# Performance work log

Hardware: AMD Instinct MI355X
Metric: run time of the kernel (lower is better)

Reference implementation:

```python
import jax, jax.numpy as jnp
import numpy as np

N_NODES = 100000
N_EDGES = 1600000
DIM_IN = 128
DIM_OUT = 64


def _spmm(edge_row, edge_col, edge_vals, X):
    # DAD.mm(X): sparse COO [N,N] times dense [N,d]
    # gather source features, scale by edge value, scatter-add to rows
    msgs = edge_vals[:, None] * X[edge_col]          # [E, d]
    return jax.ops.segment_sum(msgs, edge_row, num_segments=N_NODES)


def setup_inputs() -> dict:
    key = jax.random.key(0)
    k1, k2, k3, k4, k5, k6 = jax.random.split(key, 6)
    X = jax.random.normal(k1, (N_NODES, DIM_IN), dtype=jnp.float32)
    W1 = jax.random.normal(k2, (DIM_IN, DIM_IN), dtype=jnp.float32) * (1.0 / np.sqrt(DIM_IN))
    W2 = jax.random.normal(k3, (DIM_OUT, DIM_IN), dtype=jnp.float32) * (1.0 / np.sqrt(DIM_IN))
    edge_vals = jax.random.uniform(k4, (N_EDGES,), dtype=jnp.float32)
    edge_row = jax.random.randint(k5, (N_EDGES,), 0, N_NODES, dtype=jnp.int32)
    edge_col = jax.random.randint(k6, (N_EDGES,), 0, N_NODES, dtype=jnp.int32)
    return {"X": X, "W1": W1, "W2": W2, "edge_vals": edge_vals,
            "edge_row": edge_row, "edge_col": edge_col}


def reference(X, W1, W2, edge_vals, edge_row, edge_col):
    # layer 1: tanh(fc1(DAD @ X)); nn.Linear(bias=False) is x @ W.T
    h = jnp.tanh(_spmm(edge_row, edge_col, edge_vals, X) @ W1.T)
    # layer 2: tanh(fc2(DAD @ h))
    out = jnp.tanh(_spmm(edge_row, edge_col, edge_vals, h) @ W2.T)
    return out
```

## Files before the change

kernel.cpp:

```cpp
#include <hip/hip_runtime.h>
#include <hip/hip_bf16.h>
#include <hip/hip_fp16.h>

#define N_NODES 100000
#define N_EDGES 1600000
#define DIM_IN 128
#define DIM_OUT 64

#define NB 391
#define NCHUNK 391
#define CHUNK 4096
#define BCAP 5120
#define EPCAP 6144

typedef unsigned int uint;
typedef unsigned short ushort;
typedef _Float16 half8 __attribute__((ext_vector_type(8)));
typedef float f32x4 __attribute__((ext_vector_type(4)));

__device__ inline ushort f2h(float f) {
    __half h = __float2half(f);
    return *reinterpret_cast<ushort*>(&h);
}


__global__ __launch_bounds__(256) void chunk_hist_kernel(const int* __restrict__ erow,
                                                         int* __restrict__ counts, int E) {
    __shared__ int hist[NB];
    const int t = threadIdx.x, c = blockIdx.x;
    for (int b = t; b < NB; b += 256) hist[b] = 0;
    __syncthreads();
    const int eb = c * CHUNK;
#pragma unroll
    for (int i = 0; i < CHUNK / 256; ++i) {
        int e = eb + i * 256 + t;
        if (e < E) atomicAdd(&hist[erow[e] >> 8], 1);
    }
    __syncthreads();
    for (int b = t; b < NB; b += 256) counts[b * NCHUNK + c] = hist[b];
}

__global__ __launch_bounds__(512) void bucket_scan_kernel(const int* __restrict__ counts,
                                                          int* __restrict__ offnb,
                                                          int* __restrict__ tot) {
    __shared__ int s[512];
    const int b = blockIdx.x, t = threadIdx.x;
    int v = (t < NCHUNK) ? counts[b * NCHUNK + t] : 0;
    s[t] = v;
    __syncthreads();
#pragma unroll
    for (int o = 1; o < 512; o <<= 1) {
        int x = s[t];
        int y = (t >= o) ? s[t - o] : 0;
        __syncthreads();
        s[t] = x + y;
        __syncthreads();
    }
    if (t < NCHUNK) offnb[b * NCHUNK + t] = s[t] - v;
    if (t == 511) tot[b] = s[511];
}

__global__ __launch_bounds__(512) void base_scan_kernel(const int* __restrict__ tot,
                                                        int* __restrict__ bbase) {
    __shared__ int s[512];
    const int t = threadIdx.x;
    int v = (t < NB) ? tot[t] : 0;
    s[t] = v;
    __syncthreads();
#pragma unroll
    for (int o = 1; o < 512; o <<= 1) {
        int x = s[t];
        int y = (t >= o) ? s[t - o] : 0;
        __syncthreads();
        s[t] = x + y;
        __syncthreads();
    }
    if (t < NB) bbase[t] = s[t] - v;
    if (t == 511) bbase[NB] = s[511];
}

__global__ __launch_bounds__(512) void coarse_scatter_kernel(const int* __restrict__ erow,
                                                             const int* __restrict__ ecol,
                                                             const float* __restrict__ eval,
                                                             const int* __restrict__ offnb,
                                                             const int* __restrict__ bbase,
                                                             uint* __restrict__ keyOut,
                                                             float* __restrict__ valOut, int E) {
    __shared__ int hist[NB];
    __shared__ int segOff[NB];
    __shared__ int localOff[NB];
    __shared__ int sc[512];
    __shared__ int idxL[CHUNK];
    __shared__ int gaddrL[CHUNK];

    const int t = threadIdx.x, c = blockIdx.x;
    for (int b = t; b < NB; b += 512) {
        hist[b] = 0;
        segOff[b] = bbase[b] + offnb[b * NCHUNK + c];
    }
    __syncthreads();
    const int eb = c * CHUNK;
    uint bq[CHUNK / 512];
#pragma unroll
    for (int i = 0; i < CHUNK / 512; ++i) {
        int e = eb + i * 512 + t;
        if (e < E) {
            int b = erow[e] >> 8;
            int q = atomicAdd(&hist[b], 1);
            bq[i] = ((uint)b << 16) | (uint)q;
        } else {
            bq[i] = 0xFFFFFFFFu;
        }
    }
    __syncthreads();
    int v = (t < NB) ? hist[t] : 0;
    sc[t] = v;
    __syncthreads();
#pragma unroll
    for (int o = 1; o < 512; o <<= 1) {
        int x = sc[t];
        int y = (t >= o) ? sc[t - o] : 0;
        __syncthreads();
        sc[t] = x + y;
        __syncthreads();
    }
    if (t < NB) localOff[t] = sc[t] - v;
    __syncthreads();
#pragma unroll
    for (int i = 0; i < CHUNK / 512; ++i) {
        if (bq[i] != 0xFFFFFFFFu) {
            int b = bq[i] >> 16;
            int q = bq[i] & 0xFFFF;
            int s = localOff[b] + q;
            idxL[s] = eb + i * 512 + t;
            gaddrL[s] = segOff[b] + q;
        }
    }
    __syncthreads();
    const int m = min(CHUNK, E - eb);
    for (int s = t; s < m; s += 512) {
        int e = idxL[s];
        int g = gaddrL[s];
        keyOut[g] = ((uint)(erow[e] & 255) << 17) | (uint)ecol[e];
        valOut[g] = eval[e];
    }
}

__global__ __launch_bounds__(256) void fine_sort_kernel(const uint* __restrict__ keyOut,
                                                        const float* __restrict__ valOut,
                                                        const int* __restrict__ bbase,
                                                        int* __restrict__ row_ptr,
                                                        int* __restrict__ row_len,
                                                        int2* __restrict__ ep) {
    __shared__ uint keyL[BCAP];
    __shared__ int hist[256];
    __shared__ int offs[256];
    const int b = blockIdx.x, t = threadIdx.x;
    const int s0 = bbase[b], s1 = bbase[b + 1];
    const int m = min(s1 - s0, BCAP);
    hist[t] = 0;
    __syncthreads();
    for (int j = t; j < m; j += 256) {
        uint k = keyOut[s0 + j];
        keyL[j] = k;
        atomicAdd(&hist[k >> 17], 1);
    }
    __syncthreads();
    const int deg = hist[t];
    const int pdeg = (deg + 7) & ~7;
    offs[t] = pdeg;
    __syncthreads();
#pragma unroll
    for (int o = 1; o < 256; o <<= 1) {
        int x = offs[t];
        int y = (t >= o) ? offs[t - o] : 0;
        __syncthreads();
        offs[t] = x + y;
        __syncthreads();
    }
    const int pexcl = offs[t] - pdeg;
    const int base = b * EPCAP;
    const int row = b * 256 + t;
    if (row < N_NODES) {
        row_ptr[row] = base + pexcl;
        row_len[row] = pdeg;
    }
    hist[t] = pexcl;
    __syncthreads();
    for (int j = t; j < m; j += 256) {
        uint k = keyL[j];
        int pos = atomicAdd(&hist[k >> 17], 1);
        ep[base + pos] = make_int2((int)(k & 0x1FFFFu), __float_as_int(valOut[s0 + j]));
    }
    __syncthreads();
    for (int j = pexcl + deg; j < pexcl + pdeg; ++j)
        ep[base + j] = make_int2(0, 0);
}


__global__ __launch_bounds__(256) void cvt_f16_kernel(const float* __restrict__ in,
                                                      uint* __restrict__ outp, int n8) {
    int i = blockIdx.x * 256 + threadIdx.x;
    if (i >= n8) return;
    const float4* in4 = reinterpret_cast<const float4*>(in) + (size_t)i * 2;
    float4 a = in4[0];
    float4 b = in4[1];
    uint4 o;
    o.x = (uint)f2h(a.x) | ((uint)f2h(a.y) << 16);
    o.y = (uint)f2h(a.z) | ((uint)f2h(a.w) << 16);
    o.z = (uint)f2h(b.x) | ((uint)f2h(b.y) << 16);
    o.w = (uint)f2h(b.z) | ((uint)f2h(b.w) << 16);
    reinterpret_cast<uint4*>(outp)[i] = o;
}


template <int NOUT, bool TANH, bool AF32>
__global__ __launch_bounds__(256) void mfma_gemm_kernel(const void* __restrict__ Ain,
                                                        const uint* __restrict__ Wh,
                                                        uint* __restrict__ Out, int M) {
    constexpr int CF = NOUT / 16;
    __shared__ __align__(16) ushort sA[128 * 128];
    __shared__ __align__(16) ushort sB[NOUT * 128];

    const int t = threadIdx.x;
    const int l = t & 63;
    const int w = t >> 6;
    const int row0 = blockIdx.x * 128;
    const int lr = l & 15;
    const int lk = l >> 4;

    if (AF32) {
        const float* Af = (const float*)Ain;
#pragma unroll
        for (int i = 0; i < 16; ++i) {
            int fid = i * 256 + t;
            int row = fid >> 5, q4 = fid & 31;
            int gr = row0 + row;
            float4 v = make_float4(0.f, 0.f, 0.f, 0.f);
            if (gr < M) v = *reinterpret_cast<const float4*>(Af + (size_t)gr * 128 + q4 * 4);
            uint2 p;
            p.x = (uint)f2h(v.x) | ((uint)f2h(v.y) << 16);
            p.y = (uint)f2h(v.z) | ((uint)f2h(v.w) << 16);
            int slot = q4 >> 1;
            *reinterpret_cast<uint2*>(&sA[row * 128 + ((slot ^ (row & 7)) << 3) + (q4 & 1) * 4]) = p;
        }
    } else {
        const uint4* A4 = (const uint4*)Ain;
#pragma unroll
        for (int i = 0; i < 8; ++i) {
            int fid = i * 256 + t;
            int row = fid >> 4, slot = fid & 15;
            int gr = row0 + row;
            uint4 v = make_uint4(0, 0, 0, 0);
            if (gr < M) v = A4[(size_t)gr * 16 + slot];
            *reinterpret_cast<uint4*>(&sA[row * 128 + ((slot ^ (row & 7)) << 3)]) = v;
        }
    }
#pragma unroll
    for (int i = 0; i < NOUT / 16; ++i) {
        int fid = i * 256 + t;
        int row = fid >> 4, slot = fid & 15;
        uint4 v = reinterpret_cast<const uint4*>(Wh)[row * 16 + slot];
        *reinterpret_cast<uint4*>(&sB[row * 128 + ((slot ^ (row & 7)) << 3)]) = v;
    }
    __syncthreads();

    f32x4 acc[2][CF];
#pragma unroll
    for (int rf = 0; rf < 2; ++rf)
#pragma unroll
        for (int cf = 0; cf < CF; ++cf) acc[rf][cf] = (f32x4){0.f, 0.f, 0.f, 0.f};

    half8 aF[2][4];
#pragma unroll
    for (int rf = 0; rf < 2; ++rf) {
        int row = w * 32 + rf * 16 + lr;
#pragma unroll
        for (int kc = 0; kc < 4; ++kc) {
            int slot = kc * 4 + lk;
            aF[rf][kc] = *reinterpret_cast<const half8*>(&sA[row * 128 + ((slot ^ (row & 7)) << 3)]);
        }
    }
#pragma unroll
    for (int cf = 0; cf < CF; ++cf) {
        int col = cf * 16 + lr;
#pragma unroll
        for (int kc = 0; kc < 4; ++kc) {
            int slot = kc * 4 + lk;
            half8 bF = *reinterpret_cast<const half8*>(&sB[col * 128 + ((slot ^ (col & 7)) << 3)]);
            acc[0][cf] = __builtin_amdgcn_mfma_f32_16x16x32_f16(aF[0][kc], bF, acc[0][cf], 0, 0, 0);
            acc[1][cf] = __builtin_amdgcn_mfma_f32_16x16x32_f16(aF[1][kc], bF, acc[1][cf], 0, 0, 0);
        }
    }
    __syncthreads();

    ushort* sOut = sA;
#pragma unroll
    for (int rf = 0; rf < 2; ++rf)
#pragma unroll
        for (int cf = 0; cf < CF; ++cf)
#pragma unroll
            for (int reg = 0; reg < 4; ++reg) {
                int row = w * 32 + rf * 16 + lk * 4 + reg;
                int col = cf * 16 + lr;
                float x = acc[rf][cf][reg];
                sOut[row * NOUT + col] = f2h(TANH ? tanhf(x) : x);
            }
    __syncthreads();
    constexpr int QPR = NOUT / 8;
#pragma unroll
    for (int i = 0; i < 128 * QPR / 256; ++i) {
        int fid = i * 256 + t;
        int row = fid / QPR, q = fid % QPR;
        int gr = row0 + row;
        if (gr < M)
            reinterpret_cast<uint4*>(Out)[(size_t)gr * QPR + q] =
                *reinterpret_cast<const uint4*>(&sOut[row * NOUT + q * 8]);
    }
}


__global__ __launch_bounds__(256) void spmm1_kernel(const int2* __restrict__ ep,
                                                    const int* __restrict__ row_ptr,
                                                    const int* __restrict__ row_len,
                                                    const uint* __restrict__ T,
                                                    uint* __restrict__ Hh) {
    int wave = threadIdx.x >> 6;
    int lane = threadIdx.x & 63;
    int r = blockIdx.x * 4 + wave;
    if (r >= N_NODES) return;
    int beg = row_ptr[r];
    int end = beg + row_len[r];
    float a0x = 0.f, a0y = 0.f, a1x = 0.f, a1y = 0.f;
    for (int e = beg; e < end; e += 8) {
        int2 cv[8];
        uint xu[8];
#pragma unroll
        for (int i = 0; i < 8; ++i) cv[i] = ep[e + i];
#pragma unroll
        for (int i = 0; i < 8; ++i) xu[i] = T[(size_t)cv[i].x * 64 + lane];
#pragma unroll
        for (int i = 0; i < 8; ++i) {
            float v = __int_as_float(cv[i].y);
            __half2 h2 = *reinterpret_cast<__half2*>(&xu[i]);
            float2 f = __half22float2(h2);
            if (i & 1) { a1x += v * f.x; a1y += v * f.y; }
            else       { a0x += v * f.x; a0y += v * f.y; }
        }
    }
    Hh[(size_t)r * 64 + lane] =
        (uint)f2h(tanhf(a0x + a1x)) | ((uint)f2h(tanhf(a0y + a1y)) << 16);
}


__global__ __launch_bounds__(256) void spmm2_kernel(const int2* __restrict__ ep,
                                                    const int* __restrict__ row_ptr,
                                                    const int* __restrict__ row_len,
                                                    const ushort* __restrict__ Ph,
                                                    float* __restrict__ out) {
    int wave = threadIdx.x >> 6;
    int lane = threadIdx.x & 63;
    int r = blockIdx.x * 4 + wave;
    if (r >= N_NODES) return;
    int beg = row_ptr[r];
    int end = beg + row_len[r];
    float acc0 = 0.f, acc1 = 0.f;
    for (int e = beg; e < end; e += 8) {
        int2 cv[8];
        ushort xu[8];
#pragma unroll
        for (int i = 0; i < 8; ++i) cv[i] = ep[e + i];
#pragma unroll
        for (int i = 0; i < 8; ++i) xu[i] = Ph[(size_t)cv[i].x * 64 + lane];
#pragma unroll
        for (int i = 0; i < 8; ++i) {
            float v = __int_as_float(cv[i].y);
            __half h = *reinterpret_cast<__half*>(&xu[i]);
            float x = __half2float(h);
            if (i & 1) acc1 += v * x;
            else       acc0 += v * x;
        }
    }
    out[(size_t)r * DIM_OUT + lane] = tanhf(acc0 + acc1);
}


extern "C" void kernel_launch(void* const* d_in, const int* in_sizes, int n_in,
                              void* d_out, int out_size, void* d_ws, size_t ws_size,
                              hipStream_t stream) {
    const float* X = (const float*)d_in[0];
    const float* W1 = (const float*)d_in[1];
    const float* W2 = (const float*)d_in[2];
    const float* evals = (const float*)d_in[3];
    const int* erow = (const int*)d_in[4];
    const int* ecol = (const int*)d_in[5];
    float* out = (float*)d_out;

    const int N = N_NODES;
    const int E = N_EDGES;

    char* ws = (char*)d_ws;
    size_t off = 0;
    auto alloc = [&](size_t bytes) {
        size_t o = off;
        off = (off + bytes + 255) & ~(size_t)255;
        return o;
    };
    size_t o_counts = alloc((size_t)NB * NCHUNK * 4);
    size_t o_offnb = alloc((size_t)NB * NCHUNK * 4);
    size_t o_tot = alloc((size_t)NB * 4);
    size_t o_bbase = alloc((size_t)(NB + 1) * 4);
    size_t o_rowptr = alloc((size_t)N * 4);
    size_t o_rowlen = alloc((size_t)N * 4);
    size_t o_ep = alloc((size_t)NB * EPCAP * 8);
    size_t o_key = alloc((size_t)E * 4);
    size_t o_val = alloc((size_t)E * 4);
    size_t o_xw1 = alloc((size_t)N * 64 * 4);
    size_t o_hh = alloc((size_t)N * 64 * 4);
    size_t o_ph = alloc((size_t)N * 32 * 4);
    size_t o_w1h = alloc((size_t)128 * 64 * 4);
    size_t o_w2h = alloc((size_t)64 * 64 * 4);
    (void)ws_size;

    int* counts = (int*)(ws + o_counts);
    int* offnb = (int*)(ws + o_offnb);
    int* tot = (int*)(ws + o_tot);
    int* bbase = (int*)(ws + o_bbase);
    int* row_ptr = (int*)(ws + o_rowptr);
    int* row_len = (int*)(ws + o_rowlen);
    int2* ep = (int2*)(ws + o_ep);
    uint* keyOut = (uint*)(ws + o_key);
    float* valOut = (float*)(ws + o_val);
    uint* XW1h = (uint*)(ws + o_xw1);
    uint* Hh = (uint*)(ws + o_hh);
    uint* Ph = (uint*)(ws + o_ph);
    uint* W1h = (uint*)(ws + o_w1h);
    uint* W2h = (uint*)(ws + o_w2h);

    const int gemm_grid = (N + 127) / 128;
    const int spmm_grid = (N + 3) / 4;

    cvt_f16_kernel<<<8, 256, 0, stream>>>(W1, W1h, 128 * 128 / 8);
    cvt_f16_kernel<<<4, 256, 0, stream>>>(W2, W2h, 64 * 128 / 8);
    mfma_gemm_kernel<128, false, true><<<gemm_grid, 256, 0, stream>>>(X, W1h, XW1h, N);

    chunk_hist_kernel<<<NCHUNK, 256, 0, stream>>>(erow, counts, E);
    bucket_scan_kernel<<<NB, 512, 0, stream>>>(counts, offnb, tot);
    base_scan_kernel<<<1, 512, 0, stream>>>(tot, bbase);
    coarse_scatter_kernel<<<NCHUNK, 512, 0, stream>>>(erow, ecol, evals, offnb, bbase,
                                                      keyOut, valOut, E);
    fine_sort_kernel<<<NB, 256, 0, stream>>>(keyOut, valOut, bbase, row_ptr, row_len, ep);

    spmm1_kernel<<<spmm_grid, 256, 0, stream>>>(ep, row_ptr, row_len, XW1h, Hh);
    mfma_gemm_kernel<64, false, false><<<gemm_grid, 256, 0, stream>>>(Hh, W2h, Ph, N);
    spmm2_kernel<<<spmm_grid, 256, 0, stream>>>(ep, row_ptr, row_len, (const ushort*)Ph, out);
}
```

Before: 208.1 us.

## Fuse first SpMM with second-layer GEMM and merge weight conversions

The first SpMM kernel now processes 16 rows per block, writes the tanh'd rows into shared memory, and immediately multiplies them by W2 with MFMA. This removes the Hh intermediate round trip to global memory and one GEMM launch. The two weight-conversion kernels are merged into one launch, and the GEMM is specialised to the 128-output case. Each block now also loads all of W2 into shared memory, and the larger blocks may lower occupancy or balance load less evenly across rows of different degree.

```diff
diff --git a/kernel.cpp b/kernel.cpp
--- a/kernel.cpp
+++ b/kernel.cpp
@@ -198,11 +198,18 @@
 }
 
 
-__global__ __launch_bounds__(256) void cvt_f16_kernel(const float* __restrict__ in,
-                                                      uint* __restrict__ outp, int n8) {
+__global__ __launch_bounds__(256) void cvt_weights_kernel(const float* __restrict__ W1,
+                                                          const float* __restrict__ W2,
+                                                          uint* __restrict__ W1h,
+                                                          uint* __restrict__ W2h) {
     int i = blockIdx.x * 256 + threadIdx.x;
-    if (i >= n8) return;
-    const float4* in4 = reinterpret_cast<const float4*>(in) + (size_t)i * 2;
+    const float* in;
+    uint* outp;
+    int j;
+    if (i < 2048) { in = W1; outp = W1h; j = i; }
+    else if (i < 3072) { in = W2; outp = W2h; j = i - 2048; }
+    else return;
+    const float4* in4 = reinterpret_cast<const float4*>(in) + (size_t)j * 2;
     float4 a = in4[0];
     float4 b = in4[1];
     uint4 o;
@@ -210,17 +217,15 @@
     o.y = (uint)f2h(a.z) | ((uint)f2h(a.w) << 16);
     o.z = (uint)f2h(b.x) | ((uint)f2h(b.y) << 16);
     o.w = (uint)f2h(b.z) | ((uint)f2h(b.w) << 16);
-    reinterpret_cast<uint4*>(outp)[i] = o;
-}
-
-
-template <int NOUT, bool TANH, bool AF32>
-__global__ __launch_bounds__(256) void mfma_gemm_kernel(const void* __restrict__ Ain,
-                                                        const uint* __restrict__ Wh,
-                                                        uint* __restrict__ Out, int M) {
-    constexpr int CF = NOUT / 16;
+    reinterpret_cast<uint4*>(outp)[j] = o;
+}
+
+
+__global__ __launch_bounds__(256) void mfma_gemm128_kernel(const float* __restrict__ Af,
+                                                           const uint* __restrict__ Wh,
+                                                           uint* __restrict__ Out, int M) {
     __shared__ __align__(16) ushort sA[128 * 128];
-    __shared__ __align__(16) ushort sB[NOUT * 128];
+    __shared__ __align__(16) ushort sB[128 * 128];
 
     const int t = threadIdx.x;
     const int l = t & 63;
@@ -229,35 +234,21 @@
     const int lr = l & 15;
     const int lk = l >> 4;
 
-    if (AF32) {
-        const float* Af = (const float*)Ain;
-#pragma unroll
-        for (int i = 0; i < 16; ++i) {
-            int fid = i * 256 + t;
-            int row = fid >> 5, q4 = fid & 31;
-            int gr = row0 + row;
-            float4 v = make_float4(0.f, 0.f, 0.f, 0.f);
-            if (gr < M) v = *reinterpret_cast<const float4*>(Af + (size_t)gr * 128 + q4 * 4);
-            uint2 p;
-            p.x = (uint)f2h(v.x) | ((uint)f2h(v.y) << 16);
-            p.y = (uint)f2h(v.z) | ((uint)f2h(v.w) << 16);
-            int slot = q4 >> 1;
-            *reinterpret_cast<uint2*>(&sA[row * 128 + ((slot ^ (row & 7)) << 3) + (q4 & 1) * 4]) = p;
-        }
-    } else {
-        const uint4* A4 = (const uint4*)Ain;
-#pragma unroll
-        for (int i = 0; i < 8; ++i) {
-            int fid = i * 256 + t;
-            int row = fid >> 4, slot = fid & 15;
-            int gr = row0 + row;
-            uint4 v = make_uint4(0, 0, 0, 0);
-            if (gr < M) v = A4[(size_t)gr * 16 + slot];
-            *reinterpret_cast<uint4*>(&sA[row * 128 + ((slot ^ (row & 7)) << 3)]) = v;
-        }
-    }
-#pragma unroll
-    for (int i = 0; i < NOUT / 16; ++i) {
+#pragma unroll
+    for (int i = 0; i < 16; ++i) {
+        int fid = i * 256 + t;
+        int row = fid >> 5, q4 = fid & 31;
+        int gr = row0 + row;
+        float4 v = make_float4(0.f, 0.f, 0.f, 0.f);
+        if (gr < M) v = *reinterpret_cast<const float4*>(Af + (size_t)gr * 128 + q4 * 4);
+        uint2 p;
+        p.x = (uint)f2h(v.x) | ((uint)f2h(v.y) << 16);
+        p.y = (uint)f2h(v.z) | ((uint)f2h(v.w) << 16);
+        int slot = q4 >> 1;
+        *reinterpret_cast<uint2*>(&sA[row * 128 + ((slot ^ (row & 7)) << 3) + (q4 & 1) * 4]) = p;
+    }
+#pragma unroll
+    for (int i = 0; i < 8; ++i) {
         int fid = i * 256 + t;
         int row = fid >> 4, slot = fid & 15;
         uint4 v = reinterpret_cast<const uint4*>(Wh)[row * 16 + slot];
@@ -265,11 +256,11 @@
     }
     __syncthreads();
 
-    f32x4 acc[2][CF];
+    f32x4 acc[2][8];
 #pragma unroll
     for (int rf = 0; rf < 2; ++rf)
 #pragma unroll
-        for (int cf = 0; cf < CF; ++cf) acc[rf][cf] = (f32x4){0.f, 0.f, 0.f, 0.f};
+        for (int cf = 0; cf < 8; ++cf) acc[rf][cf] = (f32x4){0.f, 0.f, 0.f, 0.f};
 
     half8 aF[2][4];
 #pragma unroll
@@ -282,7 +273,7 @@
         }
     }
 #pragma unroll
-    for (int cf = 0; cf < CF; ++cf) {
+    for (int cf = 0; cf < 8; ++cf) {
         int col = cf * 16 + lr;
 #pragma unroll
         for (int kc = 0; kc < 4; ++kc) {
@@ -298,58 +289,106 @@
 #pragma unroll
     for (int rf = 0; rf < 2; ++rf)
 #pragma unroll
-        for (int cf = 0; cf < CF; ++cf)
+        for (int cf = 0; cf < 8; ++cf)
 #pragma unroll
             for (int reg = 0; reg < 4; ++reg) {
                 int row = w * 32 + rf * 16 + lk * 4 + reg;
                 int col = cf * 16 + lr;
-                float x = acc[rf][cf][reg];
-                sOut[row * NOUT + col] = f2h(TANH ? tanhf(x) : x);
+                sOut[row * 128 + col] = f2h(acc[rf][cf][reg]);
             }
     __syncthreads();
-    constexpr int QPR = NOUT / 8;
-#pragma unroll
-    for (int i = 0; i < 128 * QPR / 256; ++i) {
+#pragma unroll
+    for (int i = 0; i < 8; ++i) {
         int fid = i * 256 + t;
-        int row = fid / QPR, q = fid % QPR;
+        int row = fid >> 4, q = fid & 15;
         int gr = row0 + row;
         if (gr < M)
-            reinterpret_cast<uint4*>(Out)[(size_t)gr * QPR + q] =
-                *reinterpret_cast<const uint4*>(&sOut[row * NOUT + q * 8]);
-    }
-}
-
-
-__global__ __launch_bounds__(256) void spmm1_kernel(const int2* __restrict__ ep,
-                                                    const int* __restrict__ row_ptr,
-                                                    const int* __restrict__ row_len,
-                                                    const uint* __restrict__ T,
-                                                    uint* __restrict__ Hh) {
-    int wave = threadIdx.x >> 6;
-    int lane = threadIdx.x & 63;
-    int r = blockIdx.x * 4 + wave;
-    if (r >= N_NODES) return;
-    int beg = row_ptr[r];
-    int end = beg + row_len[r];
-    float a0x = 0.f, a0y = 0.f, a1x = 0.f, a1y = 0.f;
-    for (int e = beg; e < end; e += 8) {
-        int2 cv[8];
-        uint xu[8];
-#pragma unroll
-        for (int i = 0; i < 8; ++i) cv[i] = ep[e + i];
-#pragma unroll
-        for (int i = 0; i < 8; ++i) xu[i] = T[(size_t)cv[i].x * 64 + lane];
-#pragma unroll
-        for (int i = 0; i < 8; ++i) {
-            float v = __int_as_float(cv[i].y);
-            __half2 h2 = *reinterpret_cast<__half2*>(&xu[i]);
-            float2 f = __half22float2(h2);
-            if (i & 1) { a1x += v * f.x; a1y += v * f.y; }
-            else       { a0x += v * f.x; a0y += v * f.y; }
-        }
-    }
-    Hh[(size_t)r * 64 + lane] =
-        (uint)f2h(tanhf(a0x + a1x)) | ((uint)f2h(tanhf(a0y + a1y)) << 16);
+            reinterpret_cast<uint4*>(Out)[(size_t)gr * 16 + q] =
+                *reinterpret_cast<const uint4*>(&sOut[row * 128 + q * 8]);
+    }
+}
+
+
+__global__ __launch_bounds__(256) void spmm1_fused_kernel(const int2* __restrict__ ep,
+                                                          const int* __restrict__ row_ptr,
+                                                          const int* __restrict__ row_len,
+                                                          const uint* __restrict__ T,
+                                                          const uint* __restrict__ W2h,
+                                                          uint* __restrict__ Ph, int M) {
+    __shared__ __align__(16) ushort sH[16 * 128];
+    __shared__ __align__(16) ushort sW2[64 * 128];
+    __shared__ __align__(16) ushort sP[16 * 64];
+
+    const int t = threadIdx.x;
+    const int l = t & 63;
+    const int w = t >> 6;
+    const int lr = l & 15;
+    const int lk = l >> 4;
+    const int row0 = blockIdx.x * 16;
+
+#pragma unroll
+    for (int i = 0; i < 4; ++i) {
+        int fid = i * 256 + t;
+        int row = fid >> 4, slot = fid & 15;
+        uint4 v = reinterpret_cast<const uint4*>(W2h)[row * 16 + slot];
+        *reinterpret_cast<uint4*>(&sW2[row * 128 + ((slot ^ (row & 7)) << 3)]) = v;
+    }
+
+    uint* sHu = reinterpret_cast<uint*>(sH);
+#pragma unroll
+    for (int rr = 0; rr < 4; ++rr) {
+        const int lrow = w * 4 + rr;
+        const int r = row0 + lrow;
+        float a0x = 0.f, a0y = 0.f, a1x = 0.f, a1y = 0.f;
+        if (r < M) {
+            int beg = row_ptr[r];
+            int end = beg + row_len[r];
+            for (int e = beg; e < end; e += 8) {
+                int2 cv[8];
+                uint xu[8];
+#pragma unroll
+                for (int i = 0; i < 8; ++i) cv[i] = ep[e + i];
+#pragma unroll
+                for (int i = 0; i < 8; ++i) xu[i] = T[(size_t)cv[i].x * 64 + l];
+#pragma unroll
+                for (int i = 0; i < 8; ++i) {
+                    float v = __int_as_float(cv[i].y);
+                    __half2 h2 = *reinterpret_cast<__half2*>(&xu[i]);
+                    float2 f = __half22float2(h2);
+                    if (i & 1) { a1x += v * f.x; a1y += v * f.y; }
+                    else       { a0x += v * f.x; a0y += v * f.y; }
+                }
+            }
+        }
+        uint hv = (uint)f2h(tanhf(a0x + a1x)) | ((uint)f2h(tanhf(a0y + a1y)) << 16);
+        int slot = l >> 2;
+        sHu[lrow * 64 + ((slot ^ (lrow & 7)) << 2) + (l & 3)] = hv;
+    }
+    __syncthreads();
+
+    f32x4 acc = (f32x4){0.f, 0.f, 0.f, 0.f};
+    const int col = w * 16 + lr;
+#pragma unroll
+    for (int kc = 0; kc < 4; ++kc) {
+        int slot = kc * 4 + lk;
+        half8 aF = *reinterpret_cast<const half8*>(&sH[lr * 128 + ((slot ^ (lr & 7)) << 3)]);
+        half8 bF = *reinterpret_cast<const half8*>(&sW2[col * 128 + ((slot ^ (col & 7)) << 3)]);
+        acc = __builtin_amdgcn_mfma_f32_16x16x32_f16(aF, bF, acc, 0, 0, 0);
+    }
+#pragma unroll
+    for (int reg = 0; reg < 4; ++reg) {
+        int row = lk * 4 + reg;
+        sP[row * 64 + col] = f2h(acc[reg]);
+    }
+    __syncthreads();
+
+    if (t < 128) {
+        int row = t >> 3, q = t & 7;
+        int gr = row0 + row;
+        if (gr < M)
+            reinterpret_cast<uint4*>(Ph)[(size_t)gr * 8 + q] =
+                *reinterpret_cast<const uint4*>(&sP[row * 64 + q * 8]);
+    }
 }
 
 
@@ -416,7 +455,6 @@
     size_t o_key = alloc((size_t)E * 4);
     size_t o_val = alloc((size_t)E * 4);
     size_t o_xw1 = alloc((size_t)N * 64 * 4);
-    size_t o_hh = alloc((size_t)N * 64 * 4);
     size_t o_ph = alloc((size_t)N * 32 * 4);
     size_t o_w1h = alloc((size_t)128 * 64 * 4);
     size_t o_w2h = alloc((size_t)64 * 64 * 4);
@@ -432,17 +470,16 @@
     uint* keyOut = (uint*)(ws + o_key);
     float* valOut = (float*)(ws + o_val);
     uint* XW1h = (uint*)(ws + o_xw1);
-    uint* Hh = (uint*)(ws + o_hh);
     uint* Ph = (uint*)(ws + o_ph);
     uint* W1h = (uint*)(ws + o_w1h);
     uint* W2h = (uint*)(ws + o_w2h);
 
     const int gemm_grid = (N + 127) / 128;
-    const int spmm_grid = (N + 3) / 4;
-
-    cvt_f16_kernel<<<8, 256, 0, stream>>>(W1, W1h, 128 * 128 / 8);
-    cvt_f16_kernel<<<4, 256, 0, stream>>>(W2, W2h, 64 * 128 / 8);
-    mfma_gemm_kernel<128, false, true><<<gemm_grid, 256, 0, stream>>>(X, W1h, XW1h, N);
+    const int spmm2_grid = (N + 3) / 4;
+    const int fused_grid = (N + 15) / 16;
+
+    cvt_weights_kernel<<<12, 256, 0, stream>>>(W1, W2, W1h, W2h);
+    mfma_gemm128_kernel<<<gemm_grid, 256, 0, stream>>>(X, W1h, XW1h, N);
 
     chunk_hist_kernel<<<NCHUNK, 256, 0, stream>>>(erow, counts, E);
     bucket_scan_kernel<<<NB, 512, 0, stream>>>(counts, offnb, tot);
@@ -451,7 +488,6 @@
                                                       keyOut, valOut, E);
     fine_sort_kernel<<<NB, 256, 0, stream>>>(keyOut, valOut, bbase, row_ptr, row_len, ep);
 
-    spmm1_kernel<<<spmm_grid, 256, 0, stream>>>(ep, row_ptr, row_len, XW1h, Hh);
-    mfma_gemm_kernel<64, false, false><<<gemm_grid, 256, 0, stream>>>(Hh, W2h, Ph, N);
-    spmm2_kernel<<<spmm_grid, 256, 0, stream>>>(ep, row_ptr, row_len, (const ushort*)Ph, out);
-}
+    spmm1_fused_kernel<<<fused_grid, 256, 0, stream>>>(ep, row_ptr, row_len, XW1h, W2h, Ph, N);
+    spmm2_kernel<<<spmm2_grid, 256, 0, stream>>>(ep, row_ptr, row_len, (const ushort*)Ph, out);
+}
```

Result: faster. 200.0 us (-3.9%).
